# Performance work log

Measured on AMD Instinct MI355X. Metric: run time of the kernel, lower is better.

Reference implementation:

```python
import jax, jax.numpy as jnp
import numpy as np

B, SEQ, C_IN, F, K = 32, 16384, 64, 64, 9

def setup_inputs() -> dict:
    key = jax.random.key(0)
    k1, k2 = jax.random.split(key)
    x = jax.random.normal(k1, (B, SEQ, C_IN), dtype=jnp.float32)
    w = jax.random.normal(k2, (F, K, C_IN), dtype=jnp.float32) * 0.05  # mimics random_normal_initializer stddev
    b = jnp.zeros((F,), dtype=jnp.float32)
    return {"x": x, "w": w, "b": b}

def reference(x, w, b):
    # Faithful math: out[bt, t, f] = sum_{k,c} w[f,k,c] * x[bt, t+k, c] + b[f]
    # (VALID padding, stride 1). Expressed as an efficient conv instead of the
    # original unrolled loop + giant stacked intermediate.
    kernel = jnp.transpose(w, (1, 2, 0))  # [K, C_in, F] for WIO layout
    out = jax.lax.conv_general_dilated(
        x, kernel,
        window_strides=(1,),
        padding='VALID',
        dimension_numbers=('NWC', 'WIO', 'NWC'),
    )  # [B, SEQ-K+1, F]
    return out + b[None, None, :]
```

## Files before the change

kernel.cpp:

```cpp
#include <hip/hip_runtime.h>
#include <hip/hip_bf16.h>

#define T_IN   16384
#define T_OUT  16376
#define CIN    64
#define NF     64
#define KT     9
#define NB     32
#define TILE   128
#define ROWS   (TILE + KT - 1)
#define LDS_STRIDE 72
#define TILES_PER_BATCH 128
#define NTILES (NB * TILES_PER_BATCH)
#define NBLOCKS 512
#define TILE_ITERS (NTILES / NBLOCKS)

typedef __bf16 bf16x8 __attribute__((ext_vector_type(8)));
typedef unsigned short u16x8 __attribute__((ext_vector_type(8)));
typedef unsigned short u16x4 __attribute__((ext_vector_type(4)));
typedef float f32x16 __attribute__((ext_vector_type(16)));

__device__ __forceinline__ unsigned short f2bf(float f) {
    unsigned u = __builtin_bit_cast(unsigned, f);
    u += 0x7FFFu + ((u >> 16) & 1u);
    return (unsigned short)(u >> 16);
}

__global__ __launch_bounds__(256, 2) void conv1d_mfma_kernel(
    const float* __restrict__ x,
    const float* __restrict__ w,
    const float* __restrict__ b,
    float* __restrict__ out)
{
    __shared__ __attribute__((aligned(16))) unsigned short ldsX[ROWS * LDS_STRIDE];

    const int tid  = threadIdx.x;
    const int lane = tid & 63;
    const int wv   = tid >> 6;
    const int half = lane >> 5;
    const int l31  = lane & 31;
    const int fh   = wv & 1;
    const int rh   = wv >> 1;
    const int fbase = fh * 32;
    const int rbase = rh * 64;
    const int fcol  = fbase + l31;

    bf16x8 Bf[KT][4];
#pragma unroll
    for (int k = 0; k < KT; ++k) {
#pragma unroll
        for (int s = 0; s < 4; ++s) {
            const float* wp = w + (size_t)fcol * (KT * CIN) + k * CIN + s * 16 + half * 8;
            const float4 w0 = *(const float4*)(wp);
            const float4 w1 = *(const float4*)(wp + 4);
            u16x8 t;
            t[0] = f2bf(w0.x); t[1] = f2bf(w0.y); t[2] = f2bf(w0.z); t[3] = f2bf(w0.w);
            t[4] = f2bf(w1.x); t[5] = f2bf(w1.y); t[6] = f2bf(w1.z); t[7] = f2bf(w1.w);
            Bf[k][s] = __builtin_bit_cast(bf16x8, t);
        }
    }
    const float bias = b[fcol];

    for (int it = 0; it < TILE_ITERS; ++it) {
        const int g  = blockIdx.x * TILE_ITERS + it;
        const int bb = g >> 7;
        const int t0 = (g & 127) << 7;

        for (int i = tid; i < ROWS * 16; i += 256) {
            const int r  = i >> 4;
            const int cg = i & 15;
            int gr = t0 + r;
            gr = gr < (T_IN - 1) ? gr : (T_IN - 1);
            const float4 v = *(const float4*)(x + ((size_t)bb * T_IN + gr) * CIN + cg * 4);
            u16x4 p;
            p[0] = f2bf(v.x); p[1] = f2bf(v.y); p[2] = f2bf(v.z); p[3] = f2bf(v.w);
            *(u16x4*)&ldsX[r * LDS_STRIDE + cg * 4] = p;
        }
        __syncthreads();

        f32x16 acc0 = {0,0,0,0,0,0,0,0,0,0,0,0,0,0,0,0};
        f32x16 acc1 = {0,0,0,0,0,0,0,0,0,0,0,0,0,0,0,0};
        const int abase = (rbase + l31) * LDS_STRIDE + half * 8;
#pragma unroll
        for (int k = 0; k < KT; ++k) {
#pragma unroll
            for (int s = 0; s < 4; ++s) {
                const int off = abase + k * LDS_STRIDE + s * 16;
                bf16x8 a0 = *(const bf16x8*)&ldsX[off];
                bf16x8 a1 = *(const bf16x8*)&ldsX[off + 32 * LDS_STRIDE];
                acc0 = __builtin_amdgcn_mfma_f32_32x32x16_bf16(a0, Bf[k][s], acc0, 0, 0, 0);
                acc1 = __builtin_amdgcn_mfma_f32_32x32x16_bf16(a1, Bf[k][s], acc1, 0, 0, 0);
            }
        }

#pragma unroll
        for (int m = 0; m < 2; ++m) {
            const f32x16 A = m ? acc1 : acc0;
#pragma unroll
            for (int r = 0; r < 16; ++r) {
                const int tl = rbase + m * 32 + (r & 3) + 8 * (r >> 2) + 4 * half;
                const int tg = t0 + tl;
                if (tg < T_OUT)
                    out[((size_t)bb * T_OUT + tg) * NF + fcol] = A[r] + bias;
            }
        }
        __syncthreads();
    }
}

extern "C" void kernel_launch(void* const* d_in, const int* in_sizes, int n_in,
                              void* d_out, int out_size, void* d_ws, size_t ws_size,
                              hipStream_t stream) {
    const float* x = (const float*)d_in[0];
    const float* w = (const float*)d_in[1];
    const float* b = (const float*)d_in[2];
    float* out = (float*)d_out;
    conv1d_mfma_kernel<<<NBLOCKS, 256, 0, stream>>>(x, w, b, out);
}
```

Baseline: 295.3 us.

## Launch one block per tile and issue input loads before weight conversion

```diff
diff --git a/kernel.cpp b/kernel.cpp
--- a/kernel.cpp
+++ b/kernel.cpp
@@ -12,8 +12,6 @@
 #define LDS_STRIDE 72
 #define TILES_PER_BATCH 128
 #define NTILES (NB * TILES_PER_BATCH)
-#define NBLOCKS 512
-#define TILE_ITERS (NTILES / NBLOCKS)
 
 typedef __bf16 bf16x8 __attribute__((ext_vector_type(8)));
 typedef unsigned short u16x8 __attribute__((ext_vector_type(8)));
@@ -26,7 +24,7 @@
     return (unsigned short)(u >> 16);
 }
 
-__global__ __launch_bounds__(256, 2) void conv1d_mfma_kernel(
+__global__ __launch_bounds__(256, 4) void conv1d_mfma_kernel(
     const float* __restrict__ x,
     const float* __restrict__ w,
     const float* __restrict__ b,
@@ -41,9 +39,29 @@
     const int l31  = lane & 31;
     const int fh   = wv & 1;
     const int rh   = wv >> 1;
-    const int fbase = fh * 32;
     const int rbase = rh * 64;
-    const int fcol  = fbase + l31;
+    const int fcol  = fh * 32 + l31;
+
+    const int g  = blockIdx.x;
+    const int bb = g >> 7;
+    const int t0 = (g & 127) << 7;
+
+    float4 xv[9];
+    int    xr[9], xc[9];
+    int nst = 0;
+#pragma unroll
+    for (int i = 0; i < 9; ++i) {
+        const int u = tid + i * 256;
+        if (u < ROWS * 16) {
+            const int r  = u >> 4;
+            const int cg = u & 15;
+            int gr = t0 + r;
+            gr = gr < (T_IN - 1) ? gr : (T_IN - 1);
+            xv[i] = *(const float4*)(x + ((size_t)bb * T_IN + gr) * CIN + cg * 4);
+            xr[i] = r; xc[i] = cg;
+            ++nst;
+        }
+    }
 
     bf16x8 Bf[KT][4];
 #pragma unroll
@@ -61,50 +79,42 @@
     }
     const float bias = b[fcol];
 
-    for (int it = 0; it < TILE_ITERS; ++it) {
-        const int g  = blockIdx.x * TILE_ITERS + it;
-        const int bb = g >> 7;
-        const int t0 = (g & 127) << 7;
+#pragma unroll
+    for (int i = 0; i < 9; ++i) {
+        if (i < nst) {
+            u16x4 p;
+            p[0] = f2bf(xv[i].x); p[1] = f2bf(xv[i].y);
+            p[2] = f2bf(xv[i].z); p[3] = f2bf(xv[i].w);
+            *(u16x4*)&ldsX[xr[i] * LDS_STRIDE + xc[i] * 4] = p;
+        }
+    }
+    __syncthreads();
 
-        for (int i = tid; i < ROWS * 16; i += 256) {
-            const int r  = i >> 4;
-            const int cg = i & 15;
-            int gr = t0 + r;
-            gr = gr < (T_IN - 1) ? gr : (T_IN - 1);
-            const float4 v = *(const float4*)(x + ((size_t)bb * T_IN + gr) * CIN + cg * 4);
-            u16x4 p;
-            p[0] = f2bf(v.x); p[1] = f2bf(v.y); p[2] = f2bf(v.z); p[3] = f2bf(v.w);
-            *(u16x4*)&ldsX[r * LDS_STRIDE + cg * 4] = p;
+    f32x16 acc0 = {0,0,0,0,0,0,0,0,0,0,0,0,0,0,0,0};
+    f32x16 acc1 = {0,0,0,0,0,0,0,0,0,0,0,0,0,0,0,0};
+    const int abase = (rbase + l31) * LDS_STRIDE + half * 8;
+#pragma unroll
+    for (int k = 0; k < KT; ++k) {
+#pragma unroll
+        for (int s = 0; s < 4; ++s) {
+            const int off = abase + k * LDS_STRIDE + s * 16;
+            bf16x8 a0 = *(const bf16x8*)&ldsX[off];
+            bf16x8 a1 = *(const bf16x8*)&ldsX[off + 32 * LDS_STRIDE];
+            acc0 = __builtin_amdgcn_mfma_f32_32x32x16_bf16(a0, Bf[k][s], acc0, 0, 0, 0);
+            acc1 = __builtin_amdgcn_mfma_f32_32x32x16_bf16(a1, Bf[k][s], acc1, 0, 0, 0);
         }
-        __syncthreads();
-
-        f32x16 acc0 = {0,0,0,0,0,0,0,0,0,0,0,0,0,0,0,0};
-        f32x16 acc1 = {0,0,0,0,0,0,0,0,0,0,0,0,0,0,0,0};
-        const int abase = (rbase + l31) * LDS_STRIDE + half * 8;
-#pragma unroll
-        for (int k = 0; k < KT; ++k) {
-#pragma unroll
-            for (int s = 0; s < 4; ++s) {
-                const int off = abase + k * LDS_STRIDE + s * 16;
-                bf16x8 a0 = *(const bf16x8*)&ldsX[off];
-                bf16x8 a1 = *(const bf16x8*)&ldsX[off + 32 * LDS_STRIDE];
-                acc0 = __builtin_amdgcn_mfma_f32_32x32x16_bf16(a0, Bf[k][s], acc0, 0, 0, 0);
-                acc1 = __builtin_amdgcn_mfma_f32_32x32x16_bf16(a1, Bf[k][s], acc1, 0, 0, 0);
-            }
-        }
+    }
 
 #pragma unroll
-        for (int m = 0; m < 2; ++m) {
-            const f32x16 A = m ? acc1 : acc0;
+    for (int m = 0; m < 2; ++m) {
+        const f32x16 A = m ? acc1 : acc0;
 #pragma unroll
-            for (int r = 0; r < 16; ++r) {
-                const int tl = rbase + m * 32 + (r & 3) + 8 * (r >> 2) + 4 * half;
-                const int tg = t0 + tl;
-                if (tg < T_OUT)
-                    out[((size_t)bb * T_OUT + tg) * NF + fcol] = A[r] + bias;
-            }
+        for (int r = 0; r < 16; ++r) {
+            const int tl = rbase + m * 32 + (r & 3) + 8 * (r >> 2) + 4 * half;
+            const int tg = t0 + tl;
+            if (tg < T_OUT)
+                out[((size_t)bb * T_OUT + tg) * NF + fcol] = A[r] + bias;
         }
-        __syncthreads();
     }
 }
 
@@ -115,5 +125,5 @@
     const float* w = (const float*)d_in[1];
     const float* b = (const float*)d_in[2];
     float* out = (float*)d_out;
-    conv1d_mfma_kernel<<<NBLOCKS, 256, 0, stream>>>(x, w, b, out);
+    conv1d_mfma_kernel<<<NTILES, 256, 0, stream>>>(x, w, b, out);
 }
```

Result: slower. 601.3 us (+103.6%).
